# Performance work log

Measured on AMD Instinct MI355X. Metric: run time of the kernel, lower is better.

## Reference

```python
import jax, jax.numpy as jnp
import numpy as np

WIN = 16  # win_size == stride


def setup_inputs() -> dict:
    key = jax.random.key(0)
    k0, k1, k2 = jax.random.split(key, 3)
    B, M, D, H = 32, 2048, 512, 64  # H = input_size // time_ratio
    return {
        "x": jax.random.normal(k0, (B, M, D), dtype=jnp.float32),
        "W1": jax.random.normal(k1, (D, H), dtype=jnp.float32) / np.sqrt(D).astype(np.float32),
        "b1": jnp.zeros((H,), jnp.float32),
        "W2": jax.random.normal(k2, (H, D), dtype=jnp.float32) / np.sqrt(H).astype(np.float32),
        "b2": jnp.zeros((D,), jnp.float32),
    }


def _softsign(v):
    return v / (1.0 + jnp.abs(v))


def reference(x, W1, b1, W2, b2):
    B, M, D = x.shape
    pad_total = (-M) % WIN
    lo = pad_total // 2
    hi = pad_total - lo
    xp = jnp.pad(x, ((0, 0), (lo, hi), (0, 0)), mode="edge")
    Mp = M + pad_total
    nW = Mp // WIN
    xw = xp.reshape(B, nW, WIN, D)
    m = xw.mean(axis=2)                     # windowed mean-pool -> [B, nW, D]
    h = _softsign(jnp.einsum("bwd,dh->bwh", m, W1) + b1)
    g = jax.nn.sigmoid(_softsign(jnp.einsum("bwh,hd->bwd", h, W2) + b2))  # [B, nW, D]
    y = (xw * g[:, :, None, :]).reshape(B, Mp, D)  # broadcast gate over window
    return y[:, lo:lo + M, :]
```

## Files before the change

kernel.cpp:

```cpp
#include <hip/hip_runtime.h>
#include <cmath>


constexpr int WIN = 16;
constexpr int D   = 512;
constexpr int H   = 64;
constexpr int TPB = 256;
constexpr int NW  = 2;

__global__ __launch_bounds__(TPB) void se_block_kernel(
    const float* __restrict__ x,
    const float* __restrict__ W1,
    const float* __restrict__ b1,
    const float* __restrict__ W2,
    const float* __restrict__ b2,
    float* __restrict__ y)
{
    const int tid = threadIdx.x;
    const size_t base = (size_t)blockIdx.x * (size_t)(NW * WIN * D);
    const float4* __restrict__ xw = reinterpret_cast<const float4*>(x + base);
    float4*       __restrict__ yw = reinterpret_cast<float4*>(y + base);

    const float4* __restrict__ W1f4 = reinterpret_cast<const float4*>(W1);
    const float4* __restrict__ W2f4 = reinterpret_cast<const float4*>(W2);
    const float4* __restrict__ b2f4 = reinterpret_cast<const float4*>(b2);

    __shared__ __align__(16) char s_regionA[NW * TPB * 16];
    __shared__ __align__(16) char s_regionB[16 * NW * 16 * 16];
    __shared__ float s_h[NW][H];

    float4* s_ps = reinterpret_cast<float4*>(s_regionA);
    float4* s_gp = reinterpret_cast<float4*>(s_regionA);
    float4* s_hp = reinterpret_cast<float4*>(s_regionB);
    float4* s_g4 = reinterpret_cast<float4*>(s_regionB);

#pragma unroll
    for (int w = 0; w < NW; ++w) {
        float4 ps = make_float4(0.f, 0.f, 0.f, 0.f);
#pragma unroll
        for (int i = 0; i < 8; ++i) {
            const float4 v = xw[w * 2048 + i * TPB + tid];
            ps.x += v.x; ps.y += v.y; ps.z += v.z; ps.w += v.w;
        }
        s_ps[w * TPB + tid] = ps;
    }
    __syncthreads();

    {
        const int p  = tid >> 4;
        const int j4 = tid & 15;
        float4 acc[NW];
#pragma unroll
        for (int w = 0; w < NW; ++w) acc[w] = make_float4(0.f, 0.f, 0.f, 0.f);
#pragma unroll 2
        for (int kk4 = 0; kk4 < 8; ++kk4) {
            const int c4 = p * 8 + kk4;
            const int k  = c4 * 4;
            const float4 w0 = W1f4[(size_t)(k + 0) * 16 + j4];
            const float4 w1 = W1f4[(size_t)(k + 1) * 16 + j4];
            const float4 w2 = W1f4[(size_t)(k + 2) * 16 + j4];
            const float4 w3 = W1f4[(size_t)(k + 3) * 16 + j4];
#pragma unroll
            for (int w = 0; w < NW; ++w) {
                const float4 a = s_ps[w * TPB + c4];
                const float4 b = s_ps[w * TPB + c4 + 128];
                const float mv0 = a.x + b.x, mv1 = a.y + b.y;
                const float mv2 = a.z + b.z, mv3 = a.w + b.w;
                acc[w].x = fmaf(mv0, w0.x, acc[w].x); acc[w].y = fmaf(mv0, w0.y, acc[w].y);
                acc[w].z = fmaf(mv0, w0.z, acc[w].z); acc[w].w = fmaf(mv0, w0.w, acc[w].w);
                acc[w].x = fmaf(mv1, w1.x, acc[w].x); acc[w].y = fmaf(mv1, w1.y, acc[w].y);
                acc[w].z = fmaf(mv1, w1.z, acc[w].z); acc[w].w = fmaf(mv1, w1.w, acc[w].w);
                acc[w].x = fmaf(mv2, w2.x, acc[w].x); acc[w].y = fmaf(mv2, w2.y, acc[w].y);
                acc[w].z = fmaf(mv2, w2.z, acc[w].z); acc[w].w = fmaf(mv2, w2.w, acc[w].w);
                acc[w].x = fmaf(mv3, w3.x, acc[w].x); acc[w].y = fmaf(mv3, w3.y, acc[w].y);
                acc[w].z = fmaf(mv3, w3.z, acc[w].z); acc[w].w = fmaf(mv3, w3.w, acc[w].w);
            }
        }
        __syncthreads();
        const float sc = 1.0f / 16.0f;
#pragma unroll
        for (int w = 0; w < NW; ++w) {
            float4 v = acc[w];
            v.x *= sc; v.y *= sc; v.z *= sc; v.w *= sc;
            s_hp[(p * NW + w) * 16 + j4] = v;
        }
    }
    __syncthreads();

    if (tid < NW * H) {
        const float* s_hpf = reinterpret_cast<const float*>(s_hp);
        const int w = tid >> 6;
        const int j = tid & 63;
        float s = b1[j];
#pragma unroll
        for (int p = 0; p < 16; ++p) s += s_hpf[(p * NW + w) * H + j];
        s_h[w][j] = s / (1.0f + fabsf(s));
    }
    __syncthreads();

    {
        const float4* s_h4 = reinterpret_cast<const float4*>(&s_h[0][0]);
        const int q  = tid >> 7;
        const int d4 = tid & 127;
        float4 acc[NW];
#pragma unroll
        for (int w = 0; w < NW; ++w) acc[w] = make_float4(0.f, 0.f, 0.f, 0.f);
#pragma unroll 2
        for (int jj4 = 0; jj4 < 8; ++jj4) {
            const int jg = q * 8 + jj4;
            const int j  = jg * 4;
            const float4 w0 = W2f4[(size_t)(j + 0) * 128 + d4];
            const float4 w1 = W2f4[(size_t)(j + 1) * 128 + d4];
            const float4 w2 = W2f4[(size_t)(j + 2) * 128 + d4];
            const float4 w3 = W2f4[(size_t)(j + 3) * 128 + d4];
#pragma unroll
            for (int w = 0; w < NW; ++w) {
                const float4 hv = s_h4[w * 16 + jg];
                acc[w].x = fmaf(hv.x, w0.x, acc[w].x); acc[w].y = fmaf(hv.x, w0.y, acc[w].y);
                acc[w].z = fmaf(hv.x, w0.z, acc[w].z); acc[w].w = fmaf(hv.x, w0.w, acc[w].w);
                acc[w].x = fmaf(hv.y, w1.x, acc[w].x); acc[w].y = fmaf(hv.y, w1.y, acc[w].y);
                acc[w].z = fmaf(hv.y, w1.z, acc[w].z); acc[w].w = fmaf(hv.y, w1.w, acc[w].w);
                acc[w].x = fmaf(hv.z, w2.x, acc[w].x); acc[w].y = fmaf(hv.z, w2.y, acc[w].y);
                acc[w].z = fmaf(hv.z, w2.z, acc[w].z); acc[w].w = fmaf(hv.z, w2.w, acc[w].w);
                acc[w].x = fmaf(hv.w, w3.x, acc[w].x); acc[w].y = fmaf(hv.w, w3.y, acc[w].y);
                acc[w].z = fmaf(hv.w, w3.z, acc[w].z); acc[w].w = fmaf(hv.w, w3.w, acc[w].w);
            }
        }
        __syncthreads();
#pragma unroll
        for (int w = 0; w < NW; ++w) s_gp[(q * NW + w) * 128 + d4] = acc[w];
    }
    __syncthreads();

    {
        const int w  = tid >> 7;
        const int d4 = tid & 127;
        const float4 a  = s_gp[(0 * NW + w) * 128 + d4];
        const float4 b  = s_gp[(1 * NW + w) * 128 + d4];
        const float4 bb = b2f4[d4];
        float4 s;
        s.x = a.x + b.x + bb.x; s.y = a.y + b.y + bb.y;
        s.z = a.z + b.z + bb.z; s.w = a.w + b.w + bb.w;
        s.x = s.x / (1.0f + fabsf(s.x)); s.y = s.y / (1.0f + fabsf(s.y));
        s.z = s.z / (1.0f + fabsf(s.z)); s.w = s.w / (1.0f + fabsf(s.w));
        float4 g;
        g.x = 1.0f / (1.0f + __expf(-s.x)); g.y = 1.0f / (1.0f + __expf(-s.y));
        g.z = 1.0f / (1.0f + __expf(-s.z)); g.w = 1.0f / (1.0f + __expf(-s.w));
        __syncthreads();
        s_g4[w * 128 + d4] = g;
    }
    __syncthreads();

    {
        const int c = tid & 127;
#pragma unroll
        for (int w = 0; w < NW; ++w) {
            const float4 g = s_g4[w * 128 + c];
#pragma unroll
            for (int i = 0; i < 8; ++i) {
                const float4 v = xw[w * 2048 + i * TPB + tid];
                float4 o;
                o.x = v.x * g.x; o.y = v.y * g.y; o.z = v.z * g.z; o.w = v.w * g.w;
                yw[w * 2048 + i * TPB + tid] = o;
            }
        }
    }
}

extern "C" void kernel_launch(void* const* d_in, const int* in_sizes, int n_in,
                              void* d_out, int out_size, void* d_ws, size_t ws_size,
                              hipStream_t stream) {
    const float* x  = (const float*)d_in[0];
    const float* W1 = (const float*)d_in[1];
    const float* b1 = (const float*)d_in[2];
    const float* W2 = (const float*)d_in[3];
    const float* b2 = (const float*)d_in[4];
    float* y = (float*)d_out;

    const int n_windows = in_sizes[0] / (WIN * D);
    const int n_blocks  = n_windows / NW;
    se_block_kernel<<<dim3(n_blocks), dim3(TPB), 0, stream>>>(x, W1, b1, W2, b2, y);
}
```

Before: 65.63 us.

## Hold x tiles in registers and prefetch next window group across 4-group blocks

```diff
diff --git a/kernel.cpp b/kernel.cpp
--- a/kernel.cpp
+++ b/kernel.cpp
@@ -7,44 +7,48 @@
 constexpr int H   = 64;
 constexpr int TPB = 256;
 constexpr int NW  = 2;
-
-__global__ __launch_bounds__(TPB) void se_block_kernel(
-    const float* __restrict__ x,
-    const float* __restrict__ W1,
-    const float* __restrict__ b1,
-    const float* __restrict__ W2,
-    const float* __restrict__ b2,
-    float* __restrict__ y)
+constexpr int NG  = 4;
+constexpr int GSTRIDE = NW * WIN * D / 4;
+
+__device__ __forceinline__ void bar_lds() {
+    asm volatile("s_waitcnt lgkmcnt(0)" ::: "memory");
+    __builtin_amdgcn_s_barrier();
+    asm volatile("" ::: "memory");
+}
+
+__device__ __forceinline__ void load_group(const float4* __restrict__ xg, int tid,
+                                           float4 r[NW][8]) {
+#pragma unroll
+    for (int w = 0; w < NW; ++w)
+#pragma unroll
+        for (int i = 0; i < 8; ++i)
+            r[w][i] = xg[w * 2048 + i * TPB + tid];
+}
+
+__device__ __forceinline__ void process_group(
+    const float4 r[NW][8], float4 rnext[NW][8], const float4* __restrict__ xnext,
+    float4* __restrict__ yg,
+    const float4* __restrict__ W1f4, const float* __restrict__ b1,
+    const float4* __restrict__ W2f4, const float4* __restrict__ b2f4,
+    float4* __restrict__ sA, float4* __restrict__ s_g4, float* __restrict__ s_h,
+    int tid)
 {
-    const int tid = threadIdx.x;
-    const size_t base = (size_t)blockIdx.x * (size_t)(NW * WIN * D);
-    const float4* __restrict__ xw = reinterpret_cast<const float4*>(x + base);
-    float4*       __restrict__ yw = reinterpret_cast<float4*>(y + base);
-
-    const float4* __restrict__ W1f4 = reinterpret_cast<const float4*>(W1);
-    const float4* __restrict__ W2f4 = reinterpret_cast<const float4*>(W2);
-    const float4* __restrict__ b2f4 = reinterpret_cast<const float4*>(b2);
-
-    __shared__ __align__(16) char s_regionA[NW * TPB * 16];
-    __shared__ __align__(16) char s_regionB[16 * NW * 16 * 16];
-    __shared__ float s_h[NW][H];
-
-    float4* s_ps = reinterpret_cast<float4*>(s_regionA);
-    float4* s_gp = reinterpret_cast<float4*>(s_regionA);
-    float4* s_hp = reinterpret_cast<float4*>(s_regionB);
-    float4* s_g4 = reinterpret_cast<float4*>(s_regionB);
+    float4* s_ps = sA;
+    float4* s_hp = sA;
+    float4* s_gp = sA;
 
 #pragma unroll
     for (int w = 0; w < NW; ++w) {
-        float4 ps = make_float4(0.f, 0.f, 0.f, 0.f);
-#pragma unroll
-        for (int i = 0; i < 8; ++i) {
-            const float4 v = xw[w * 2048 + i * TPB + tid];
-            ps.x += v.x; ps.y += v.y; ps.z += v.z; ps.w += v.w;
+        float4 ps = r[w][0];
+#pragma unroll
+        for (int i = 1; i < 8; ++i) {
+            ps.x += r[w][i].x; ps.y += r[w][i].y; ps.z += r[w][i].z; ps.w += r[w][i].w;
         }
         s_ps[w * TPB + tid] = ps;
     }
-    __syncthreads();
+    bar_lds();
+
+    if (xnext != nullptr) load_group(xnext, tid, rnext);
 
     {
         const int p  = tid >> 4;
@@ -76,7 +80,7 @@
                 acc[w].z = fmaf(mv3, w3.z, acc[w].z); acc[w].w = fmaf(mv3, w3.w, acc[w].w);
             }
         }
-        __syncthreads();
+        bar_lds();
         const float sc = 1.0f / 16.0f;
 #pragma unroll
         for (int w = 0; w < NW; ++w) {
@@ -85,7 +89,7 @@
             s_hp[(p * NW + w) * 16 + j4] = v;
         }
     }
-    __syncthreads();
+    bar_lds();
 
     if (tid < NW * H) {
         const float* s_hpf = reinterpret_cast<const float*>(s_hp);
@@ -94,12 +98,12 @@
         float s = b1[j];
 #pragma unroll
         for (int p = 0; p < 16; ++p) s += s_hpf[(p * NW + w) * H + j];
-        s_h[w][j] = s / (1.0f + fabsf(s));
-    }
-    __syncthreads();
-
-    {
-        const float4* s_h4 = reinterpret_cast<const float4*>(&s_h[0][0]);
+        s_h[w * H + j] = s / (1.0f + fabsf(s));
+    }
+    bar_lds();
+
+    {
+        const float4* s_h4 = reinterpret_cast<const float4*>(s_h);
         const int q  = tid >> 7;
         const int d4 = tid & 127;
         float4 acc[NW];
@@ -126,11 +130,10 @@
                 acc[w].z = fmaf(hv.w, w3.z, acc[w].z); acc[w].w = fmaf(hv.w, w3.w, acc[w].w);
             }
         }
-        __syncthreads();
 #pragma unroll
         for (int w = 0; w < NW; ++w) s_gp[(q * NW + w) * 128 + d4] = acc[w];
     }
-    __syncthreads();
+    bar_lds();
 
     {
         const int w  = tid >> 7;
@@ -146,10 +149,9 @@
         float4 g;
         g.x = 1.0f / (1.0f + __expf(-s.x)); g.y = 1.0f / (1.0f + __expf(-s.y));
         g.z = 1.0f / (1.0f + __expf(-s.z)); g.w = 1.0f / (1.0f + __expf(-s.w));
-        __syncthreads();
         s_g4[w * 128 + d4] = g;
     }
-    __syncthreads();
+    bar_lds();
 
     {
         const int c = tid & 127;
@@ -158,13 +160,47 @@
             const float4 g = s_g4[w * 128 + c];
 #pragma unroll
             for (int i = 0; i < 8; ++i) {
-                const float4 v = xw[w * 2048 + i * TPB + tid];
                 float4 o;
-                o.x = v.x * g.x; o.y = v.y * g.y; o.z = v.z * g.z; o.w = v.w * g.w;
-                yw[w * 2048 + i * TPB + tid] = o;
+                o.x = r[w][i].x * g.x; o.y = r[w][i].y * g.y;
+                o.z = r[w][i].z * g.z; o.w = r[w][i].w * g.w;
+                yg[w * 2048 + i * TPB + tid] = o;
             }
         }
     }
+}
+
+__global__ __launch_bounds__(TPB, 2) void se_persist_kernel(
+    const float* __restrict__ x,
+    const float* __restrict__ W1,
+    const float* __restrict__ b1,
+    const float* __restrict__ W2,
+    const float* __restrict__ b2,
+    float* __restrict__ y)
+{
+    const int tid = threadIdx.x;
+    const size_t base = (size_t)blockIdx.x * (size_t)(NG * NW * WIN * D);
+    const float4* __restrict__ xw = reinterpret_cast<const float4*>(x + base);
+    float4*       __restrict__ yw = reinterpret_cast<float4*>(y + base);
+
+    const float4* __restrict__ W1f4 = reinterpret_cast<const float4*>(W1);
+    const float4* __restrict__ W2f4 = reinterpret_cast<const float4*>(W2);
+    const float4* __restrict__ b2f4 = reinterpret_cast<const float4*>(b2);
+
+    __shared__ __align__(16) float4 sA[NW * TPB];
+    __shared__ __align__(16) float4 s_g4[NW * 128];
+    __shared__ float s_h[NW * H];
+
+    float4 rA[NW][8], rB[NW][8];
+
+    load_group(xw, tid, rA);
+    process_group(rA, rB, xw + 1 * GSTRIDE, yw,
+                  W1f4, b1, W2f4, b2f4, sA, s_g4, s_h, tid);
+    process_group(rB, rA, xw + 2 * GSTRIDE, yw + 1 * GSTRIDE,
+                  W1f4, b1, W2f4, b2f4, sA, s_g4, s_h, tid);
+    process_group(rA, rB, xw + 3 * GSTRIDE, yw + 2 * GSTRIDE,
+                  W1f4, b1, W2f4, b2f4, sA, s_g4, s_h, tid);
+    process_group(rB, rA, nullptr, yw + 3 * GSTRIDE,
+                  W1f4, b1, W2f4, b2f4, sA, s_g4, s_h, tid);
 }
 
 extern "C" void kernel_launch(void* const* d_in, const int* in_sizes, int n_in,
@@ -178,6 +214,6 @@
     float* y = (float*)d_out;
 
     const int n_windows = in_sizes[0] / (WIN * D);
-    const int n_blocks  = n_windows / NW;
-    se_block_kernel<<<dim3(n_blocks), dim3(TPB), 0, stream>>>(x, W1, b1, W2, b2, y);
-}
+    const int n_blocks  = n_windows / (NG * NW);
+    se_persist_kernel<<<dim3(n_blocks), dim3(TPB), 0, stream>>>(x, W1, b1, W2, b2, y);
+}
```

New measurement: 62.35 us. -5.0%, faster.
